# Optimization experiments

Measured on AMD Instinct MI355X. Metric: run time of the kernel, lower is better.

The kernel has to match this reference:

```python
import jax, jax.numpy as jnp
import numpy as np

B, T, F, H, E, CTX = 64, 400, 80, 256, 256, 20


def setup_inputs() -> dict:
    ks = iter(jax.random.split(jax.random.key(0), 40))

    def p(shape):
        return jax.random.normal(next(ks), shape, jnp.float32) * 0.1

    inp = {"x": p((B, T, F))}
    inp["emb_W"], inp["emb_b"] = p((E, F)), p((E,))
    for name, din, dh in [("e1", F, H), ("e2", H, H), ("e3", H, H),
                          ("d1", 2 * E, H), ("d2", H, H), ("d3", H, F)]:
        inp[name + "_Wih"] = p((4 * dh, din))
        inp[name + "_Whh"] = p((4 * dh, dh))
        inp[name + "_b"] = p((4 * dh,))  # fused b_ih + b_hh
    inp["key_W"], inp["key_b"] = p((E, H)), p((E,))
    inp["val_W"], inp["val_b"] = p((E, H)), p((E,))
    inp["epoch"] = 5  # unused when isTrain=False (no teacher forcing)
    return inp


def _lstm(xin, hc, Wih, Whh, b):
    h, c = hc
    g = xin @ Wih.T + h @ Whh.T + b
    i, f, gg, o = jnp.split(g, 4, axis=-1)  # torch gate order i,f,g,o
    c = jax.nn.sigmoid(f) * c + jax.nn.sigmoid(i) * jnp.tanh(gg)
    h = jax.nn.sigmoid(o) * jnp.tanh(c)
    return (h, c)


def _forward(x, emb_W, emb_b, e1_Wih, e1_Whh, e1_b, e2_Wih, e2_Whh, e2_b,
             e3_Wih, e3_Whh, e3_b, d1_Wih, d1_Whh, d1_b, d2_Wih, d2_Whh, d2_b,
             d3_Wih, d3_Whh, d3_b, key_W, key_b, val_W, val_b):
    Bb = x.shape[0]
    z = lambda d: (jnp.zeros((Bb, d), x.dtype), jnp.zeros((Bb, d), x.dtype))

    def encoder(enc, xin):
        e1, e2, e3 = enc
        e1 = _lstm(xin, e1, e1_Wih, e1_Whh, e1_b)
        e2 = _lstm(e1[0], e2, e2_Wih, e2_Whh, e2_b)
        e3 = _lstm(e2[0], e3, e3_Wih, e3_Whh, e3_b)
        k = e3[0] @ key_W.T + key_b
        v = e3[0] @ val_W.T + val_b
        return (e1, e2, e3), k, v

    def decoder(dec, emb, ctx):
        d1, d2, d3 = dec
        din = jnp.concatenate([emb, ctx], axis=-1)  # [B, 2E]
        d1 = _lstm(din, d1, d1_Wih, d1_Whh, d1_b)
        d2 = _lstm(d1[0], d2, d2_Wih, d2_Whh, d2_b)
        d3 = _lstm(d2[0], d3, d3_Wih, d3_Whh, d3_b)
        return (d1, d2, d3)

    # phase 1: encoder warmup over steps 0..CTX-1
    def p1(enc, xt):
        enc, k, v = encoder(enc, xt)
        return enc, (k, v)

    enc, (ks_, vs_) = jax.lax.scan(p1, (z(H), z(H), z(H)),
                                   jnp.swapaxes(x[:, :CTX], 0, 1))
    kbuf = jnp.swapaxes(ks_, 0, 1)  # [B, CTX, E]: keys for steps 0..CTX-1
    vbuf = jnp.swapaxes(vs_, 0, 1)

    # step i == CTX: first decoder step; context = current value (values[-1])
    enc, k20, v20 = encoder(enc, x[:, CTX])
    kbuf = jnp.concatenate([kbuf[:, 1:], k20[:, None]], axis=1)
    vbuf = jnp.concatenate([vbuf[:, 1:], v20[:, None]], axis=1)
    emb = x[:, CTX - 1] @ emb_W.T + emb_b
    dec = decoder((z(H), z(H), z(F)), emb, v20)
    out20 = dec[2][0]  # [B, F]

    def p2(carry, _):
        enc, dec, kbuf, vbuf, last = carry
        enc, k, v = encoder(enc, last)           # encoder_input = prev decoder out
        emb = last @ emb_W.T + emb_b             # embedding of prev decoder out
        q = dec[1][0]                            # decoder2 hidden from prev step
        attn = jax.nn.softmax(jnp.einsum('bke,be->bk', kbuf, q), axis=-1)
        ctx = jnp.einsum('bk,bke->be', attn, vbuf)
        dec = decoder(dec, emb, ctx)
        kbuf = jnp.concatenate([kbuf[:, 1:], k[:, None]], axis=1)
        vbuf = jnp.concatenate([vbuf[:, 1:], v[:, None]], axis=1)
        out = dec[2][0]
        return (enc, dec, kbuf, vbuf, out), out

    _, outs = jax.lax.scan(p2, (enc, dec, kbuf, vbuf, out20), None,
                           length=T - CTX - 1)
    # [B, T-CTX, F] = [B, 380, 80]
    return jnp.concatenate([out20[:, None], jnp.swapaxes(outs, 0, 1)], axis=1)


def reference(x, emb_W, emb_b, e1_Wih, e1_Whh, e1_b, e2_Wih, e2_Whh, e2_b,
              e3_Wih, e3_Whh, e3_b, d1_Wih, d1_Whh, d1_b, d2_Wih, d2_Whh, d2_b,
              d3_Wih, d3_Whh, d3_b, key_W, key_b, val_W, val_b, epoch):
    return _forward(x, emb_W, emb_b, e1_Wih, e1_Whh, e1_b, e2_Wih, e2_Whh, e2_b,
                    e3_Wih, e3_Whh, e3_b, d1_Wih, d1_Whh, d1_b, d2_Wih, d2_Whh,
                    d2_b, d3_Wih, d3_Whh, d3_b, key_W, key_b, val_W, val_b)
```

## Files before the change

### kernel.cpp

```cpp
#include <hip/hip_runtime.h>

typedef short bf16x8 __attribute__((ext_vector_type(8)));
typedef float f32x4 __attribute__((ext_vector_type(4)));

#define DEV static __device__ __forceinline__
#define SCOPE_AGENT __HIP_MEMORY_SCOPE_AGENT

DEV unsigned short f2bf(float f) {
  unsigned u = __float_as_uint(f);
  unsigned r = u + 0x7fffu + ((u >> 16) & 1u);
  return (unsigned short)(r >> 16);
}
DEV float bf2f(unsigned short h) { return __uint_as_float(((unsigned)h) << 16); }
DEV void f2hilo(float f, unsigned short& hi, unsigned short& lo) {
  hi = f2bf(f);
  lo = f2bf(f - bf2f(hi));
}
DEV float sigm(float x) { return 1.f / (1.f + __expf(-x)); }
DEV float tanh_(float x) {
  x = fminf(15.f, fmaxf(-15.f, x));
  float e = __expf(2.f * x);
  return (e - 1.f) / (e + 1.f);
}

DEV void st_sc_u16(unsigned short* p, unsigned short v) {
  __hip_atomic_store(p, v, __ATOMIC_RELAXED, SCOPE_AGENT);
}
DEV void st_sc_f32(float* p, float v) {
  __hip_atomic_store(p, v, __ATOMIC_RELAXED, SCOPE_AGENT);
}
DEV void st_sc_u64(unsigned long long* p, unsigned long long v) {
  __hip_atomic_store(p, v, __ATOMIC_RELAXED, SCOPE_AGENT);
}
DEV unsigned long long ld_sc_u64(const unsigned long long* p) {
  return __hip_atomic_load((unsigned long long*)p, __ATOMIC_RELAXED, SCOPE_AGENT);
}
DEV unsigned ld_sc_u32(const unsigned* p) {
  return __hip_atomic_load((unsigned*)p, __ATOMIC_RELAXED, SCOPE_AGENT);
}
DEV void vm_drain() { asm volatile("s_waitcnt vmcnt(0)" ::: "memory"); }

constexpr size_t WE1 = 1024 * 352, WE2 = 1024 * 512, WE3 = 1024 * 512,
                 WD1 = 1024 * 768, WD2 = 1024 * 512, WD3 = 320 * 352,
                 WKEY = 256 * 256, WVAL = 256 * 256, WEMB = 256 * 96;
constexpr size_t E1HI = 0, E1LO = E1HI + WE1, E2HI = E1LO + WE1, E2LO = E2HI + WE2,
                 E3HI = E2LO + WE2, E3LO = E3HI + WE3, D1HI = E3LO + WE3, D1LO = D1HI + WD1,
                 D2HI = D1LO + WD1, D2LO = D2HI + WD2, D3HI = D2LO + WD2, D3LO = D3HI + WD3,
                 KHI = D3LO + WD3, KLO = KHI + WKEY, VHI = KLO + WKEY, VLO = VHI + WVAL,
                 EMHI = VLO + WVAL, EMLO = EMHI + WEMB, WTOT = EMLO + WEMB;

constexpr size_t XPAD_ELEMS = (size_t)400 * 64 * 96;
constexpr size_t XPAD_HI_B = WTOT * 2;
constexpr size_t XPAD_LO_B = XPAD_HI_B + XPAD_ELEMS * 2;
constexpr size_t STATE_B = XPAD_LO_B + XPAD_ELEMS * 2;

constexpr size_t H256_SZB = (size_t)2 * 2 * 64 * 256 * 2;
constexpr size_t HE1 = 0, HE2 = H256_SZB, HE3 = 2 * H256_SZB, HD1 = 3 * H256_SZB,
                 HD2 = 4 * H256_SZB;
constexpr size_t HLAST = 5 * H256_SZB;
constexpr size_t HLAST_SZB = (size_t)2 * 2 * 64 * 96 * 2;
constexpr size_t BARO = HLAST + HLAST_SZB;
constexpr size_t STATE_BYTES = BARO + 9 * 400 * 4 + 64;

constexpr size_t RINGK_B = STATE_B + STATE_BYTES;
constexpr size_t RING_SZ = (size_t)22 * 64 * 256 * 4;
constexpr size_t RINGV_B = RINGK_B + RING_SZ;
constexpr size_t CTXH_B = RINGV_B + RING_SZ;
constexpr size_t CTXL_B = CTXH_B + (size_t)64 * 256 * 2;
constexpr size_t D1BP_B = CTXL_B + (size_t)64 * 256 * 2;
constexpr size_t WS_NEED = D1BP_B + 4096;

#define LE1 0
#define LE2 1
#define LE3 2
#define LKS 3
#define LAT 5
#define LD1 6
#define LD2 7
#define LD3 8

constexpr int NWG = 59;
constexpr int WGS = 256;

__global__ void prep_w(const float* __restrict__ wih, int din, const float* __restrict__ whh,
                       int dh, int rows, int dinp, int kp, unsigned short* __restrict__ whi,
                       unsigned short* __restrict__ wlo) {
  size_t idx = (size_t)blockIdx.x * 256 + threadIdx.x;
  size_t tot = (size_t)rows * kp;
  if (idx >= tot) return;
  int j = (int)(idx / kp), k = (int)(idx % kp);
  float v = 0.f;
  if (k < dinp) {
    if (k < din) v = wih[(size_t)j * din + k];
  } else {
    int k2 = k - dinp;
    if (k2 < dh) v = whh[(size_t)j * dh + k2];
  }
  unsigned short hi, lo;
  f2hilo(v, hi, lo);
  whi[idx] = hi;
  wlo[idx] = lo;
}

__global__ void prep_d1_w(const float* __restrict__ wih, const float* __restrict__ whh,
                          const float* __restrict__ embW, unsigned short* __restrict__ whi,
                          unsigned short* __restrict__ wlo) {
  size_t idx = (size_t)blockIdx.x * 256 + threadIdx.x;
  constexpr size_t tot = (size_t)1024 * 608;
  if (idx >= tot) return;
  int j = (int)(idx / 608), f = (int)(idx % 608);
  float v = 0.f;
  if (f < 96) {
    if (f < 80) {
      const float* wr = wih + (size_t)j * 512;
#pragma unroll 4
      for (int m = 0; m < 256; m++) v += wr[m] * embW[(size_t)m * 80 + f];
    }
  } else if (f < 352) {
    v = wih[(size_t)j * 512 + 256 + (f - 96)];
  } else {
    v = whh[(size_t)j * 256 + (f - 352)];
  }
  unsigned short hi, lo;
  f2hilo(v, hi, lo);
  whi[idx] = hi;
  wlo[idx] = lo;
}

__global__ void prep_d1_bias(const float* __restrict__ wih, const float* __restrict__ embb,
                             const float* __restrict__ d1b, float* __restrict__ out) {
  int j = blockIdx.x * 256 + threadIdx.x;
  if (j >= 1024) return;
  float v = d1b[j];
  const float* wr = wih + (size_t)j * 512;
#pragma unroll 4
  for (int m = 0; m < 256; m++) v += wr[m] * embb[m];
  out[j] = v;
}

__global__ void prep_x(const float* __restrict__ x, unsigned short* __restrict__ xh,
                       unsigned short* __restrict__ xl) {
  size_t idx = (size_t)blockIdx.x * 256 + threadIdx.x;
  if (idx >= XPAD_ELEMS) return;
  int t = (int)(idx / 6144), rbf = (int)(idx % 6144), b = rbf / 96, f = rbf % 96;
  float v = (f < 80) ? x[(size_t)b * 32000 + (size_t)t * 80 + f] : 0.f;
  unsigned short hi, lo;
  f2hilo(v, hi, lo);
  xh[idx] = hi;
  xl[idx] = lo;
}


template <int COLS, int STRIDE>
DEV void copy_hl(unsigned short* lds, const unsigned short* hi, const unsigned short* lo,
                 int tid) {
  constexpr int CU64 = COLS / 4;
  constexpr int PER = 64 * CU64;
  constexpr int TOT = PER * 2;
  constexpr int loOff = 64 * STRIDE;
  for (int base = 0; base < TOT; base += WGS * 32) {
    unsigned long long v[32];
    int dst[32];
#pragma unroll
    for (int u = 0; u < 32; u++) {
      int i = base + u * WGS + tid;
      dst[u] = -1;
      if (i < TOT) {
        int pl = (i >= PER) ? 1 : 0;
        int j = pl ? (i - PER) : i;
        int row = j / CU64, cc = j - row * CU64;
        const unsigned long long* s = (const unsigned long long*)(pl ? lo : hi);
        v[u] = ld_sc_u64(s + j);
        dst[u] = (pl ? loOff : 0) + row * STRIDE + ((cc * 4) ^ ((row & 7) << 3));
      }
    }
#pragma unroll
    for (int u = 0; u < 32; u++)
      if (dst[u] >= 0) *(unsigned long long*)(lds + dst[u]) = v[u];
  }
}

DEV void mfma3(f32x4& acc, bf16x8 ah, bf16x8 al, bf16x8 bh, bf16x8 bl) {
  acc = __builtin_amdgcn_mfma_f32_16x16x32_bf16(ah, bh, acc, 0, 0, 0);
  acc = __builtin_amdgcn_mfma_f32_16x16x32_bf16(al, bh, acc, 0, 0, 0);
  acc = __builtin_amdgcn_mfma_f32_16x16x32_bf16(ah, bl, acc, 0, 0, 0);
}

DEV void zacc44(f32x4 (&a)[4][4]) {
#pragma unroll
  for (int g = 0; g < 4; g++)
#pragma unroll
    for (int m = 0; m < 4; m++) a[g][m] = f32x4{0.f, 0.f, 0.f, 0.f};
}

template <int STRIDE>
DEV void mfma_range(const unsigned short* lds, int lane, int ut, int H,
                    const unsigned short* __restrict__ Whi,
                    const unsigned short* __restrict__ Wlo, int Kp, int kwOff, int kbLo,
                    int kbHi, f32x4 (&acc)[4][4]) {
  const int col = lane & 15, kg = lane >> 4;
  constexpr int loOff = 64 * STRIDE;
  for (int kb = kbLo; kb < kbHi; kb++) {
    const int ka = kb * 32 + kg * 8;
    bf16x8 ah[4], al[4];
#pragma unroll
    for (int m = 0; m < 4; m++) {
      int row = m * 16 + col;
      int off = row * STRIDE + (ka ^ ((row & 7) << 3));
      ah[m] = *(const bf16x8*)(lds + off);
      al[m] = *(const bf16x8*)(lds + loOff + off);
    }
#pragma unroll
    for (int g = 0; g < 4; g++) {
      size_t wr = (size_t)(g * H + ut * 16 + col) * Kp + kwOff + ka;
      bf16x8 bh = *(const bf16x8*)(Whi + wr);
      bf16x8 bl = *(const bf16x8*)(Wlo + wr);
#pragma unroll
      for (int m = 0; m < 4; m++) mfma3(acc[g][m], ah[m], al[m], bh, bl);
    }
  }
}

template <int COLS, int STRIDE>
DEV void chunk_pass(unsigned short* lds, const unsigned short* hi, const unsigned short* lo,
                    int tid, int lane, int ut, int utActive, int H,
                    const unsigned short* __restrict__ Whi,
                    const unsigned short* __restrict__ Wlo, int Kp, int kwOff, int half,
                    f32x4 (&acc)[4][4]) {
  __syncthreads();
  copy_hl<COLS, STRIDE>(lds, hi, lo, tid);
  __syncthreads();
  constexpr int NKB = COLS / 32;
  const int lo_kb = half ? (NKB + 1) / 2 : 0;
  const int hi_kb = half ? NKB : (NKB + 1) / 2;
  if (utActive) mfma_range<STRIDE>(lds, lane, ut, H, Whi, Wlo, Kp, kwOff, lo_kb, hi_kb, acc);
}

DEV void reduce_pair(unsigned short* lds, int lane, int pair, int half, f32x4 (&acc)[4][4]) {
  float* red = (float*)lds;
  const int base = (pair * 64 + lane) * 68;
  __syncthreads();
  if (half) {
#pragma unroll
    for (int g = 0; g < 4; g++)
#pragma unroll
      for (int m = 0; m < 4; m++)
#pragma unroll
        for (int r = 0; r < 4; r++) red[base + (g * 4 + m) * 4 + r] = acc[g][m][r];
  }
  __syncthreads();
  if (!half) {
#pragma unroll
    for (int g = 0; g < 4; g++)
#pragma unroll
      for (int m = 0; m < 4; m++)
#pragma unroll
        for (int r = 0; r < 4; r++) acc[g][m][r] += red[base + (g * 4 + m) * 4 + r];
  }
}

DEV void cell_update(int lane, int ut, int H, int Hpad, const float* __restrict__ bias,
                     f32x4 (&acc)[4][4], float (&c)[4][4], unsigned short* hwhi,
                     unsigned short* hwlo, float* outp) {
  const int col = lane & 15, kg = lane >> 4;
  const int u = ut * 16 + col;
  const float bi = bias[u], bff = bias[H + u], bg = bias[2 * H + u], bo = bias[3 * H + u];
#pragma unroll
  for (int m = 0; m < 4; m++)
#pragma unroll
    for (int r = 0; r < 4; r++) {
      int b = m * 16 + kg * 4 + r;
      float gi = acc[0][m][r] + bi, gf = acc[1][m][r] + bff;
      float gg = acc[2][m][r] + bg, go = acc[3][m][r] + bo;
      float cn = sigm(gf) * c[m][r] + sigm(gi) * tanh_(gg);
      float hh = sigm(go) * tanh_(cn);
      c[m][r] = cn;
      unsigned short hi, lo;
      f2hilo(hh, hi, lo);
      st_sc_u16(hwhi + b * Hpad + u, hi);
      st_sc_u16(hwlo + b * Hpad + u, lo);
      if (outp) outp[(size_t)b * 30400 + u] = hh;
    }
}

DEV void spin3(const unsigned* p0, unsigned t0, const unsigned* p1, unsigned t1,
               const unsigned* p2, unsigned t2) {
  for (;;) {
    unsigned a = p0 ? ld_sc_u32(p0) : 0xFFFFFFFFu;
    unsigned b = p1 ? ld_sc_u32(p1) : 0xFFFFFFFFu;
    unsigned c = p2 ? ld_sc_u32(p2) : 0xFFFFFFFFu;
    if (a >= t0 && b >= t1 && c >= t2) return;
    __builtin_amdgcn_s_sleep(1);
  }
}

__global__ void __launch_bounds__(WGS, 1)
seq_main(const float* e1b, const float* e2b, const float* e3b, const float* d2b,
         const float* d3b, const float* keyb, const float* valb, float* dout,
         unsigned char* ws) {
  __shared__ unsigned short lds_s[32768];
  unsigned short* lds = lds_s;

  const int wg = blockIdx.x, tid = threadIdx.x;
  const int wv = tid >> 6, lane = tid & 63;
  const int pair = wv >> 1, half = wv & 1;

  unsigned short* W = (unsigned short*)ws;
  const unsigned short* xh = (const unsigned short*)(ws + XPAD_HI_B);
  const unsigned short* xl = (const unsigned short*)(ws + XPAD_LO_B);
  unsigned char* st = ws + STATE_B;
  float* ringk = (float*)(ws + RINGK_B);
  float* ringv = (float*)(ws + RINGV_B);
  unsigned short* ctxh = (unsigned short*)(ws + CTXH_B);
  unsigned short* ctxl = (unsigned short*)(ws + CTXL_B);
  const float* d1bp = (const float*)(ws + D1BP_B);
  unsigned* C = (unsigned*)(st + BARO);
  auto CNT = [&](int l, int tt) { return C + l * 400 + tt; };

  auto hb = [&](size_t off, int par, int hl, int Hpad) {
    return (unsigned short*)(st + off) + (size_t)(par * 2 + hl) * 64 * Hpad;
  };
  auto bump = [&](int l, int tt) {
    if (tid == 0) __hip_atomic_fetch_add(CNT(l, tt), 1u, __ATOMIC_RELAXED, SCOPE_AGENT);
  };

  if (wg < 8) {
    const int ut = wg * 2 + pair;
    float c[4][4] = {{0.f}};
    for (int t = 0; t < 400; ++t) {
      const int p = t & 1, q = p ^ 1;
      f32x4 acc[4][4];
      zacc44(acc);
      if (tid == 0 && t >= 1) spin3(CNT(LE1, t - 1), 8, nullptr, 0, nullptr, 0);
      chunk_pass<256, 256>(lds, hb(HE1, q, 0, 256), hb(HE1, q, 1, 256), tid, lane, ut, 1, 256,
                           W + E1HI, W + E1LO, 352, 96, half, acc);
      if (tid == 0)
        spin3(t >= 21 ? CNT(LD3, t - 1) : nullptr, 3, t >= 2 ? CNT(LE2, t - 2) : nullptr, 8,
              nullptr, 0);
      if (t <= 20)
        chunk_pass<96, 128>(lds, xh + (size_t)t * 6144, xl + (size_t)t * 6144, tid, lane, ut, 1,
                            256, W + E1HI, W + E1LO, 352, 0, half, acc);
      else
        chunk_pass<96, 128>(lds, hb(HLAST, q, 0, 96), hb(HLAST, q, 1, 96), tid, lane, ut, 1,
                            256, W + E1HI, W + E1LO, 352, 0, half, acc);
      reduce_pair(lds, lane, pair, half, acc);
      if (!half)
        cell_update(lane, ut, 256, 256, e1b, acc, c, hb(HE1, p, 0, 256), hb(HE1, p, 1, 256),
                    nullptr);
      vm_drain();
      __syncthreads();
      bump(LE1, t);
    }
  } else if (wg < 16) {
    const int ut = (wg - 8) * 2 + pair;
    float c[4][4] = {{0.f}};
    for (int t = 0; t < 400; ++t) {
      const int p = t & 1, q = p ^ 1;
      f32x4 acc[4][4];
      zacc44(acc);
      if (tid == 0 && t >= 1) spin3(CNT(LE2, t - 1), 8, nullptr, 0, nullptr, 0);
      chunk_pass<256, 256>(lds, hb(HE2, q, 0, 256), hb(HE2, q, 1, 256), tid, lane, ut, 1, 256,
                           W + E2HI, W + E2LO, 512, 256, half, acc);
      if (tid == 0)
        spin3(CNT(LE1, t), 8, t >= 2 ? CNT(LE3, t - 2) : nullptr, 8, nullptr, 0);
      chunk_pass<256, 256>(lds, hb(HE1, p, 0, 256), hb(HE1, p, 1, 256), tid, lane, ut, 1, 256,
                           W + E2HI, W + E2LO, 512, 0, half, acc);
      reduce_pair(lds, lane, pair, half, acc);
      if (!half)
        cell_update(lane, ut, 256, 256, e2b, acc, c, hb(HE2, p, 0, 256), hb(HE2, p, 1, 256),
                    nullptr);
      vm_drain();
      __syncthreads();
      bump(LE2, t);
    }
  } else if (wg < 24) {
    const int ut = (wg - 16) * 2 + pair;
    float c[4][4] = {{0.f}};
    for (int t = 0; t < 400; ++t) {
      const int p = t & 1, q = p ^ 1;
      f32x4 acc[4][4];
      zacc44(acc);
      if (tid == 0 && t >= 1) spin3(CNT(LE3, t - 1), 8, nullptr, 0, nullptr, 0);
      chunk_pass<256, 256>(lds, hb(HE3, q, 0, 256), hb(HE3, q, 1, 256), tid, lane, ut, 1, 256,
                           W + E3HI, W + E3LO, 512, 256, half, acc);
      if (tid == 0) spin3(CNT(LE2, t), 8, nullptr, 0, nullptr, 0);
      chunk_pass<256, 256>(lds, hb(HE2, p, 0, 256), hb(HE2, p, 1, 256), tid, lane, ut, 1, 256,
                           W + E3HI, W + E3LO, 512, 0, half, acc);
      reduce_pair(lds, lane, pair, half, acc);
      if (tid == 0 && t >= 1) spin3(CNT(LKS, t - 1), 16, nullptr, 0, nullptr, 0);
      __syncthreads();
      if (!half)
        cell_update(lane, ut, 256, 256, e3b, acc, c, hb(HE3, p, 0, 256), hb(HE3, p, 1, 256),
                    nullptr);
      vm_drain();
      __syncthreads();
      bump(LE3, t);
    }
  } else if (wg < 40) {
    const int b0 = (wg - 24) * 4;
    float* kvx = (float*)(lds + 8192);
    for (int t = 0; t < 400; ++t) {
      const int s = (t <= 20) ? t : t - 1;
      const int ps = s & 1;
      const bool doKV = (t != 21);
      if (doKV) {
        if (tid == 0) spin3(CNT(LE3, s), 8, nullptr, 0, nullptr, 0);
        __syncthreads();
        for (int i = tid; i < 512; i += WGS) {
          int pl = i >> 8, j = i & 255, row = j >> 6, cc = j & 63;
          const unsigned long long* srcp =
              (const unsigned long long*)hb(HE3, ps, pl, 256) + (size_t)(b0 + row) * 64 + cc;
          unsigned long long v = ld_sc_u64(srcp);
          *(unsigned long long*)(lds + pl * 4096 + row * 256 +
                                 ((cc * 4) ^ ((row & 7) << 3))) = v;
        }
        __syncthreads();
      }
      bump(LKS, t);
      if (doKV) {
        const int slot = s % 22;
        const int col = lane & 15, kg = lane >> 4;
        for (int jj = 0; jj < 8; ++jj) {
          int jt = wv * 8 + jj;
          bool isK = jt < 16;
          int j = (isK ? jt : jt - 16) * 16 + col;
          const unsigned short* Whi = W + (isK ? KHI : VHI);
          const unsigned short* Wlo = W + (isK ? KLO : VLO);
          f32x4 acc = f32x4{0.f, 0.f, 0.f, 0.f};
          for (int kb = 0; kb < 8; kb++) {
            int ka = kb * 32 + kg * 8;
            int offA = col * 256 + (ka ^ ((col & 7) << 3));
            bf16x8 ah = *(const bf16x8*)(lds + offA);
            bf16x8 al = *(const bf16x8*)(lds + 4096 + offA);
            size_t wr = (size_t)j * 256 + ka;
            bf16x8 bh = *(const bf16x8*)(Whi + wr);
            bf16x8 bl = *(const bf16x8*)(Wlo + wr);
            mfma3(acc, ah, al, bh, bl);
          }
          if (kg == 0) {
            float bj = (isK ? keyb : valb)[j];
            float* ringp = (isK ? ringk : ringv) + (size_t)slot * 64 * 256;
#pragma unroll
            for (int r = 0; r < 4; r++) {
              float v = acc[r] + bj;
              st_sc_f32(ringp + (size_t)(b0 + r) * 256 + j, v);
              kvx[r * 512 + (isK ? j : 256 + j)] = v;
            }
          }
        }
        __syncthreads();
      }
      if (t == 20) {
        float f[4];
#pragma unroll
        for (int j = 0; j < 4; j++) f[j] = kvx[wv * 512 + 256 + lane * 4 + j];
        unsigned short hi[4], lo[4];
#pragma unroll
        for (int j = 0; j < 4; j++) f2hilo(f[j], hi[j], lo[j]);
        unsigned long long ph = (unsigned long long)hi[0] | ((unsigned long long)hi[1] << 16) |
                                ((unsigned long long)hi[2] << 32) |
                                ((unsigned long long)hi[3] << 48);
        unsigned long long pl = (unsigned long long)lo[0] | ((unsigned long long)lo[1] << 16) |
                                ((unsigned long long)lo[2] << 32) |
                                ((unsigned long long)lo[3] << 48);
        st_sc_u64((unsigned long long*)(ctxh + (b0 + wv) * 256 + lane * 4), ph);
        st_sc_u64((unsigned long long*)(ctxl + (b0 + wv) * 256 + lane * 4), pl);
      } else if (t >= 21) {
        if (tid == 0) spin3(CNT(LD2, t - 1), 8, CNT(LD1, t - 1), 8, nullptr, 0);
        __syncthreads();
        const int b = b0 + wv;
        const int qp = (t & 1) ^ 1;
        const unsigned short* qh = hb(HD2, qp, 0, 256);
        const unsigned short* ql = hb(HD2, qp, 1, 256);
        unsigned long long hq = ld_sc_u64((const unsigned long long*)(qh + b * 256 + lane * 4));
        unsigned long long lq = ld_sc_u64((const unsigned long long*)(ql + b * 256 + lane * 4));
        float qv[4];
#pragma unroll
        for (int j = 0; j < 4; j++)
          qv[j] = bf2f((unsigned short)(hq >> (16 * j))) + bf2f((unsigned short)(lq >> (16 * j)));
        float sArr[20];
#pragma unroll
        for (int i = 0; i < 19; i++) {
          int slot = (t - 20 + i) % 22;
          const unsigned long long* kp =
              (const unsigned long long*)(ringk + ((size_t)slot * 64 + b) * 256 + lane * 4);
          unsigned long long k0 = ld_sc_u64(kp), k1 = ld_sc_u64(kp + 1);
          sArr[i] = __uint_as_float((unsigned)k0) * qv[0] +
                    __uint_as_float((unsigned)(k0 >> 32)) * qv[1] +
                    __uint_as_float((unsigned)k1) * qv[2] +
                    __uint_as_float((unsigned)(k1 >> 32)) * qv[3];
        }
        {
          float acc19 = 0.f;
#pragma unroll
          for (int j = 0; j < 4; j++) acc19 += kvx[wv * 512 + lane * 4 + j] * qv[j];
          sArr[19] = acc19;
        }
#pragma unroll
        for (int off = 32; off >= 1; off >>= 1)
#pragma unroll
          for (int i = 0; i < 20; i++) sArr[i] += __shfl_xor(sArr[i], off, 64);
        float mx = sArr[0];
#pragma unroll
        for (int i = 1; i < 20; i++) mx = fmaxf(mx, sArr[i]);
        float den = 0.f;
#pragma unroll
        for (int i = 0; i < 20; i++) {
          sArr[i] = __expf(sArr[i] - mx);
          den += sArr[i];
        }
        float inv = 1.f / den;
        float a0 = 0.f, a1 = 0.f, a2 = 0.f, a3 = 0.f;
#pragma unroll
        for (int i = 0; i < 19; i++) {
          int slot = (t - 20 + i) % 22;
          const unsigned long long* vp =
              (const unsigned long long*)(ringv + ((size_t)slot * 64 + b) * 256 + lane * 4);
          unsigned long long v0 = ld_sc_u64(vp), v1 = ld_sc_u64(vp + 1);
          a0 += sArr[i] * __uint_as_float((unsigned)v0);
          a1 += sArr[i] * __uint_as_float((unsigned)(v0 >> 32));
          a2 += sArr[i] * __uint_as_float((unsigned)v1);
          a3 += sArr[i] * __uint_as_float((unsigned)(v1 >> 32));
        }
        a0 += sArr[19] * kvx[wv * 512 + 256 + lane * 4 + 0];
        a1 += sArr[19] * kvx[wv * 512 + 256 + lane * 4 + 1];
        a2 += sArr[19] * kvx[wv * 512 + 256 + lane * 4 + 2];
        a3 += sArr[19] * kvx[wv * 512 + 256 + lane * 4 + 3];
        float f[4] = {a0 * inv, a1 * inv, a2 * inv, a3 * inv};
        unsigned short hi[4], lo[4];
#pragma unroll
        for (int j = 0; j < 4; j++) f2hilo(f[j], hi[j], lo[j]);
        unsigned long long ph = (unsigned long long)hi[0] | ((unsigned long long)hi[1] << 16) |
                                ((unsigned long long)hi[2] << 32) |
                                ((unsigned long long)hi[3] << 48);
        unsigned long long pl = (unsigned long long)lo[0] | ((unsigned long long)lo[1] << 16) |
                                ((unsigned long long)lo[2] << 32) |
                                ((unsigned long long)lo[3] << 48);
        st_sc_u64((unsigned long long*)(ctxh + b * 256 + lane * 4), ph);
        st_sc_u64((unsigned long long*)(ctxl + b * 256 + lane * 4), pl);
      }
      vm_drain();
      __syncthreads();
      bump(LAT, t);
    }
  } else if (wg < 48) {
    const int ut = (wg - 40) * 2 + pair;
    float c[4][4] = {{0.f}};
    for (int t = 20; t < 400; ++t) {
      const int p = t & 1, q = p ^ 1;
      f32x4 acc[4][4];
      zacc44(acc);
      if (tid == 0 && t >= 21) spin3(CNT(LD1, t - 1), 8, nullptr, 0, nullptr, 0);
      chunk_pass<256, 256>(lds, hb(HD1, q, 0, 256), hb(HD1, q, 1, 256), tid, lane, ut, 1, 256,
                           W + D1HI, W + D1LO, 608, 352, half, acc);
      if (tid == 0 && t >= 21) spin3(CNT(LD3, t - 1), 3, nullptr, 0, nullptr, 0);
      if (t == 20)
        chunk_pass<96, 128>(lds, xh + (size_t)19 * 6144, xl + (size_t)19 * 6144, tid, lane, ut,
                            1, 256, W + D1HI, W + D1LO, 608, 0, half, acc);
      else
        chunk_pass<96, 128>(lds, hb(HLAST, q, 0, 96), hb(HLAST, q, 1, 96), tid, lane, ut, 1,
                            256, W + D1HI, W + D1LO, 608, 0, half, acc);
      if (tid == 0) spin3(CNT(LAT, t), 16, nullptr, 0, nullptr, 0);
      chunk_pass<256, 256>(lds, ctxh, ctxl, tid, lane, ut, 1, 256, W + D1HI, W + D1LO, 608, 96,
                           half, acc);
      reduce_pair(lds, lane, pair, half, acc);
      if (!half)
        cell_update(lane, ut, 256, 256, d1bp, acc, c, hb(HD1, p, 0, 256), hb(HD1, p, 1, 256),
                    nullptr);
      vm_drain();
      __syncthreads();
      bump(LD1, t);
    }
  } else if (wg < 56) {
    const int ut = (wg - 48) * 2 + pair;
    float c[4][4] = {{0.f}};
    for (int t = 20; t < 400; ++t) {
      const int p = t & 1, q = p ^ 1;
      f32x4 acc[4][4];
      zacc44(acc);
      if (tid == 0 && t >= 21) spin3(CNT(LD2, t - 1), 8, nullptr, 0, nullptr, 0);
      chunk_pass<256, 256>(lds, hb(HD2, q, 0, 256), hb(HD2, q, 1, 256), tid, lane, ut, 1, 256,
                           W + D2HI, W + D2LO, 512, 256, half, acc);
      if (tid == 0) spin3(CNT(LD1, t), 8, nullptr, 0, nullptr, 0);
      chunk_pass<256, 256>(lds, hb(HD1, p, 0, 256), hb(HD1, p, 1, 256), tid, lane, ut, 1, 256,
                           W + D2HI, W + D2LO, 512, 0, half, acc);
      reduce_pair(lds, lane, pair, half, acc);
      if (!half)
        cell_update(lane, ut, 256, 256, d2b, acc, c, hb(HD2, p, 0, 256), hb(HD2, p, 1, 256),
                    nullptr);
      vm_drain();
      __syncthreads();
      bump(LD2, t);
    }
  } else {
    const int ut = (wg - 56) * 2 + pair;
    const int utActive = (ut < 5) ? 1 : 0;
    float c[4][4] = {{0.f}};
    for (int t = 20; t < 400; ++t) {
      const int p = t & 1, q = p ^ 1;
      f32x4 acc[4][4];
      zacc44(acc);
      if (tid == 0 && t >= 21) spin3(CNT(LD3, t - 1), 3, nullptr, 0, nullptr, 0);
      chunk_pass<96, 128>(lds, hb(HLAST, q, 0, 96), hb(HLAST, q, 1, 96), tid, lane, ut, utActive,
                          80, W + D3HI, W + D3LO, 352, 256, half, acc);
      if (tid == 0) spin3(CNT(LD2, t), 8, nullptr, 0, nullptr, 0);
      chunk_pass<256, 256>(lds, hb(HD2, p, 0, 256), hb(HD2, p, 1, 256), tid, lane, ut, utActive,
                           80, W + D3HI, W + D3LO, 352, 0, half, acc);
      reduce_pair(lds, lane, pair, half, acc);
      if (!half && utActive)
        cell_update(lane, ut, 80, 96, d3b, acc, c, hb(HLAST, p, 0, 96), hb(HLAST, p, 1, 96),
                    dout + (size_t)(t - 20) * 80);
      vm_drain();
      __syncthreads();
      bump(LD3, t);
    }
  }
}

extern "C" void kernel_launch(void* const* d_in, const int* in_sizes, int n_in, void* d_out,
                              int out_size, void* d_ws, size_t ws_size, hipStream_t stream) {
  if (ws_size < WS_NEED) return;

  const float* x = (const float*)d_in[0];
  const float* embW = (const float*)d_in[1];
  const float* embB = (const float*)d_in[2];
  const float* e1Wih = (const float*)d_in[3];
  const float* e1Whh = (const float*)d_in[4];
  const float* e1B = (const float*)d_in[5];
  const float* e2Wih = (const float*)d_in[6];
  const float* e2Whh = (const float*)d_in[7];
  const float* e2B = (const float*)d_in[8];
  const float* e3Wih = (const float*)d_in[9];
  const float* e3Whh = (const float*)d_in[10];
  const float* e3B = (const float*)d_in[11];
  const float* d1Wih = (const float*)d_in[12];
  const float* d1Whh = (const float*)d_in[13];
  const float* d1B = (const float*)d_in[14];
  const float* d2Wih = (const float*)d_in[15];
  const float* d2Whh = (const float*)d_in[16];
  const float* d2B = (const float*)d_in[17];
  const float* d3Wih = (const float*)d_in[18];
  const float* d3Whh = (const float*)d_in[19];
  const float* d3B = (const float*)d_in[20];
  const float* keyW = (const float*)d_in[21];
  const float* keyB = (const float*)d_in[22];
  const float* valW = (const float*)d_in[23];
  const float* valB = (const float*)d_in[24];

  unsigned char* ws = (unsigned char*)d_ws;
  unsigned short* W = (unsigned short*)ws;
  float* doutf = (float*)d_out;

  auto launch_w = [&](const float* wih, int din, const float* whh, int dh, int rows, int dinp,
                      int kp, size_t offhi, size_t offlo) {
    size_t tot = (size_t)rows * kp;
    int blocks = (int)((tot + 255) / 256);
    prep_w<<<blocks, 256, 0, stream>>>(wih, din, whh, dh, rows, dinp, kp, W + offhi, W + offlo);
  };
  launch_w(e1Wih, 80, e1Whh, 256, 1024, 96, 352, E1HI, E1LO);
  launch_w(e2Wih, 256, e2Whh, 256, 1024, 256, 512, E2HI, E2LO);
  launch_w(e3Wih, 256, e3Whh, 256, 1024, 256, 512, E3HI, E3LO);
  launch_w(d2Wih, 256, d2Whh, 256, 1024, 256, 512, D2HI, D2LO);
  launch_w(d3Wih, 256, d3Whh, 80, 320, 256, 352, D3HI, D3LO);
  launch_w(keyW, 256, nullptr, 0, 256, 256, 256, KHI, KLO);
  launch_w(valW, 256, nullptr, 0, 256, 256, 256, VHI, VLO);
  {
    size_t tot = (size_t)1024 * 608;
    prep_d1_w<<<(int)((tot + 255) / 256), 256, 0, stream>>>(d1Wih, d1Whh, embW, W + D1HI,
                                                            W + D1LO);
    prep_d1_bias<<<4, 256, 0, stream>>>(d1Wih, embB, d1B, (float*)(ws + D1BP_B));
  }
  prep_x<<<(int)((XPAD_ELEMS + 255) / 256), 256, 0, stream>>>(
      x, (unsigned short*)(ws + XPAD_HI_B), (unsigned short*)(ws + XPAD_LO_B));
  hipMemsetAsync(ws + STATE_B, 0, STATE_BYTES, stream);

  seq_main<<<dim3(NWG), dim3(WGS), 0, stream>>>(e1B, e2B, e3B, d2B, d3B, keyB, valB, doutf, ws);
}
```

Baseline: 17.10 ms.

## Fuse key/value projection partials into encoder-3 workgroups and double-buffer context

Encoder-3 workgroups now stage their new hidden slice in LDS, write it out with 64-bit stores, and compute partial key/value projections over their own 32 hidden units into a double-buffered partial buffer. The attention workgroups then only sum eight partials plus bias into the K/V ring instead of running a separate projection stage with its own LKS barrier. The context buffer is double-buffered by step parity, so attention no longer has to wait on decoder-1 before overwriting it. This shortens the serial dependency chain per timestep, at the cost of extra global traffic for the partials and more work inside the encoder-3 critical path.

```diff
diff --git a/kernel.cpp b/kernel.cpp
--- a/kernel.cpp
+++ b/kernel.cpp
@@ -2,6 +2,7 @@
 
 typedef short bf16x8 __attribute__((ext_vector_type(8)));
 typedef float f32x4 __attribute__((ext_vector_type(4)));
+typedef unsigned long long u64;
 
 #define DEV static __device__ __forceinline__
 #define SCOPE_AGENT __HIP_MEMORY_SCOPE_AGENT
@@ -29,11 +30,11 @@
 DEV void st_sc_f32(float* p, float v) {
   __hip_atomic_store(p, v, __ATOMIC_RELAXED, SCOPE_AGENT);
 }
-DEV void st_sc_u64(unsigned long long* p, unsigned long long v) {
+DEV void st_sc_u64(u64* p, u64 v) {
   __hip_atomic_store(p, v, __ATOMIC_RELAXED, SCOPE_AGENT);
 }
-DEV unsigned long long ld_sc_u64(const unsigned long long* p) {
-  return __hip_atomic_load((unsigned long long*)p, __ATOMIC_RELAXED, SCOPE_AGENT);
+DEV u64 ld_sc_u64(const u64* p) {
+  return __hip_atomic_load((u64*)p, __ATOMIC_RELAXED, SCOPE_AGENT);
 }
 DEV unsigned ld_sc_u32(const unsigned* p) {
   return __hip_atomic_load((unsigned*)p, __ATOMIC_RELAXED, SCOPE_AGENT);
@@ -66,14 +67,15 @@
 constexpr size_t RING_SZ = (size_t)22 * 64 * 256 * 4;
 constexpr size_t RINGV_B = RINGK_B + RING_SZ;
 constexpr size_t CTXH_B = RINGV_B + RING_SZ;
-constexpr size_t CTXL_B = CTXH_B + (size_t)64 * 256 * 2;
-constexpr size_t D1BP_B = CTXL_B + (size_t)64 * 256 * 2;
-constexpr size_t WS_NEED = D1BP_B + 4096;
+constexpr size_t CTXL_B = CTXH_B + (size_t)2 * 64 * 256 * 2;
+constexpr size_t D1BP_B = CTXL_B + (size_t)2 * 64 * 256 * 2;
+constexpr size_t P_B = D1BP_B + 4096;
+constexpr size_t P_SZ = (size_t)2 * 8 * 64 * 512 * 4;
+constexpr size_t WS_NEED = P_B + P_SZ;
 
 #define LE1 0
 #define LE2 1
 #define LE3 2
-#define LKS 3
 #define LAT 5
 #define LD1 6
 #define LD2 7
@@ -81,6 +83,7 @@
 
 constexpr int NWG = 59;
 constexpr int WGS = 256;
+constexpr int HSTG = 20480;
 
 __global__ void prep_w(const float* __restrict__ wih, int din, const float* __restrict__ whh,
                        int dh, int rows, int dinp, int kp, unsigned short* __restrict__ whi,
@@ -159,7 +162,7 @@
   constexpr int TOT = PER * 2;
   constexpr int loOff = 64 * STRIDE;
   for (int base = 0; base < TOT; base += WGS * 32) {
-    unsigned long long v[32];
+    u64 v[32];
     int dst[32];
 #pragma unroll
     for (int u = 0; u < 32; u++) {
@@ -169,14 +172,14 @@
         int pl = (i >= PER) ? 1 : 0;
         int j = pl ? (i - PER) : i;
         int row = j / CU64, cc = j - row * CU64;
-        const unsigned long long* s = (const unsigned long long*)(pl ? lo : hi);
+        const u64* s = (const u64*)(pl ? lo : hi);
         v[u] = ld_sc_u64(s + j);
         dst[u] = (pl ? loOff : 0) + row * STRIDE + ((cc * 4) ^ ((row & 7) << 3));
       }
     }
 #pragma unroll
     for (int u = 0; u < 32; u++)
-      if (dst[u] >= 0) *(unsigned long long*)(lds + dst[u]) = v[u];
+      if (dst[u] >= 0) *(u64*)(lds + dst[u]) = v[u];
   }
 }
 
@@ -283,6 +286,41 @@
     }
 }
 
+DEV void cell_update_lds40(unsigned short* hstage, int lane, int pairIdx, int ut, int H,
+                           const float* __restrict__ bias, f32x4 (&acc)[4][4],
+                           float (&c)[4][4]) {
+  const int col = lane & 15, kg = lane >> 4;
+  const int u = ut * 16 + col;
+  const int uloc = pairIdx * 16 + col;
+  const float bi = bias[u], bff = bias[H + u], bg = bias[2 * H + u], bo = bias[3 * H + u];
+#pragma unroll
+  for (int m = 0; m < 4; m++)
+#pragma unroll
+    for (int r = 0; r < 4; r++) {
+      int b = m * 16 + kg * 4 + r;
+      float gi = acc[0][m][r] + bi, gf = acc[1][m][r] + bff;
+      float gg = acc[2][m][r] + bg, go = acc[3][m][r] + bo;
+      float cn = sigm(gf) * c[m][r] + sigm(gi) * tanh_(gg);
+      float hh = sigm(go) * tanh_(cn);
+      c[m][r] = cn;
+      unsigned short hi, lo;
+      f2hilo(hh, hi, lo);
+      hstage[b * 40 + uloc] = hi;
+      hstage[2560 + b * 40 + uloc] = lo;
+    }
+}
+
+DEV void store_h40(const unsigned short* hstage, int tid, unsigned short* hwhi,
+                   unsigned short* hwlo, int u0) {
+  for (int i = tid; i < 1024; i += WGS) {
+    int pl = i >> 9;
+    int j = i & 511;
+    int b = j >> 3, cc = j & 7;
+    u64 v = *(const u64*)(hstage + pl * 2560 + b * 40 + cc * 4);
+    st_sc_u64((u64*)((pl ? hwlo : hwhi) + (size_t)b * 256 + u0) + cc, v);
+  }
+}
+
 DEV void spin3(const unsigned* p0, unsigned t0, const unsigned* p1, unsigned t1,
                const unsigned* p2, unsigned t2) {
   for (;;) {
@@ -314,6 +352,7 @@
   unsigned short* ctxh = (unsigned short*)(ws + CTXH_B);
   unsigned short* ctxl = (unsigned short*)(ws + CTXL_B);
   const float* d1bp = (const float*)(ws + D1BP_B);
+  float* Pbuf = (float*)(ws + P_B);
   unsigned* C = (unsigned*)(st + BARO);
   auto CNT = [&](int l, int tt) { return C + l * 400 + tt; };
 
@@ -375,6 +414,7 @@
     }
   } else if (wg < 24) {
     const int ut = (wg - 16) * 2 + pair;
+    const int u0 = (wg - 16) * 32;
     float c[4][4] = {{0.f}};
     for (int t = 0; t < 400; ++t) {
       const int p = t & 1, q = p ^ 1;
@@ -387,114 +427,120 @@
       chunk_pass<256, 256>(lds, hb(HE2, p, 0, 256), hb(HE2, p, 1, 256), tid, lane, ut, 1, 256,
                            W + E3HI, W + E3LO, 512, 0, half, acc);
       reduce_pair(lds, lane, pair, half, acc);
-      if (tid == 0 && t >= 1) spin3(CNT(LKS, t - 1), 16, nullptr, 0, nullptr, 0);
-      __syncthreads();
-      if (!half)
-        cell_update(lane, ut, 256, 256, e3b, acc, c, hb(HE3, p, 0, 256), hb(HE3, p, 1, 256),
-                    nullptr);
-      vm_drain();
-      __syncthreads();
-      bump(LE3, t);
-    }
-  } else if (wg < 40) {
-    const int b0 = (wg - 24) * 4;
-    float* kvx = (float*)(lds + 8192);
-    for (int t = 0; t < 400; ++t) {
-      const int s = (t <= 20) ? t : t - 1;
-      const int ps = s & 1;
-      const bool doKV = (t != 21);
-      if (doKV) {
-        if (tid == 0) spin3(CNT(LE3, s), 8, nullptr, 0, nullptr, 0);
-        __syncthreads();
-        for (int i = tid; i < 512; i += WGS) {
-          int pl = i >> 8, j = i & 255, row = j >> 6, cc = j & 63;
-          const unsigned long long* srcp =
-              (const unsigned long long*)hb(HE3, ps, pl, 256) + (size_t)(b0 + row) * 64 + cc;
-          unsigned long long v = ld_sc_u64(srcp);
-          *(unsigned long long*)(lds + pl * 4096 + row * 256 +
-                                 ((cc * 4) ^ ((row & 7) << 3))) = v;
+      if (tid == 0 && t >= 2 && t <= 22) spin3(CNT(LAT, t - 2), 16, nullptr, 0, nullptr, 0);
+      __syncthreads();
+      unsigned short* hstage = lds + HSTG;
+      if (!half) cell_update_lds40(hstage, lane, pair, ut, 256, e3b, acc, c);
+      __syncthreads();
+      store_h40(hstage, tid, hb(HE3, p, 0, 256), hb(HE3, p, 1, 256), u0);
+      {
+        const int col = lane & 15, kg = lane >> 4;
+        bf16x8 ah[4], al[4];
+#pragma unroll
+        for (int m = 0; m < 4; m++) {
+          ah[m] = *(const bf16x8*)(hstage + (m * 16 + col) * 40 + kg * 8);
+          al[m] = *(const bf16x8*)(hstage + 2560 + (m * 16 + col) * 40 + kg * 8);
         }
-        __syncthreads();
-      }
-      bump(LKS, t);
-      if (doKV) {
-        const int slot = s % 22;
-        const int col = lane & 15, kg = lane >> 4;
+        float* Pw = Pbuf + ((size_t)(t & 1) * 8 + (wg - 16)) * (64 * 512);
         for (int jj = 0; jj < 8; ++jj) {
           int jt = wv * 8 + jj;
           bool isK = jt < 16;
-          int j = (isK ? jt : jt - 16) * 16 + col;
-          const unsigned short* Whi = W + (isK ? KHI : VHI);
-          const unsigned short* Wlo = W + (isK ? KLO : VLO);
-          f32x4 acc = f32x4{0.f, 0.f, 0.f, 0.f};
-          for (int kb = 0; kb < 8; kb++) {
-            int ka = kb * 32 + kg * 8;
-            int offA = col * 256 + (ka ^ ((col & 7) << 3));
-            bf16x8 ah = *(const bf16x8*)(lds + offA);
-            bf16x8 al = *(const bf16x8*)(lds + 4096 + offA);
-            size_t wr = (size_t)j * 256 + ka;
-            bf16x8 bh = *(const bf16x8*)(Whi + wr);
-            bf16x8 bl = *(const bf16x8*)(Wlo + wr);
-            mfma3(acc, ah, al, bh, bl);
-          }
-          if (kg == 0) {
-            float bj = (isK ? keyb : valb)[j];
-            float* ringp = (isK ? ringk : ringv) + (size_t)slot * 64 * 256;
+          int jrow = (isK ? jt : jt - 16) * 16 + col;
+          size_t wr = (size_t)jrow * 256 + u0 + kg * 8;
+          bf16x8 bh = *(const bf16x8*)(W + (isK ? KHI : VHI) + wr);
+          bf16x8 bl = *(const bf16x8*)(W + (isK ? KLO : VLO) + wr);
+          f32x4 a4[4];
+#pragma unroll
+          for (int m = 0; m < 4; m++) a4[m] = f32x4{0.f, 0.f, 0.f, 0.f};
+#pragma unroll
+          for (int m = 0; m < 4; m++) mfma3(a4[m], ah[m], al[m], bh, bl);
+          int f = isK ? jrow : jrow + 256;
+#pragma unroll
+          for (int m = 0; m < 4; m++)
 #pragma unroll
             for (int r = 0; r < 4; r++) {
-              float v = acc[r] + bj;
-              st_sc_f32(ringp + (size_t)(b0 + r) * 256 + j, v);
-              kvx[r * 512 + (isK ? j : 256 + j)] = v;
+              int b2 = m * 16 + kg * 4 + r;
+              st_sc_f32(Pw + (size_t)b2 * 512 + f, a4[m][r]);
             }
+        }
+      }
+      vm_drain();
+      __syncthreads();
+      bump(LE3, t);
+    }
+  } else if (wg < 40) {
+    const int b0 = (wg - 24) * 4;
+    const int b = b0 + wv;
+    for (int t = 0; t < 400; ++t) {
+      const int s = (t <= 20) ? t : t - 1;
+      const bool doSum = (t != 21);
+      float v[8];
+      if (doSum) {
+        if (tid == 0) spin3(CNT(LE3, s), 8, nullptr, 0, nullptr, 0);
+        __syncthreads();
+        const int slot = s % 22;
+        const float* Pb = Pbuf + (size_t)(s & 1) * 8 * 64 * 512;
+        const int f0 = lane * 8;
+#pragma unroll
+        for (int j = 0; j < 8; j++)
+          v[j] = (f0 + j < 256) ? keyb[f0 + j] : valb[f0 + j - 256];
+        for (int w = 0; w < 8; w++) {
+          const u64* src = (const u64*)(Pb + ((size_t)w * 64 + b) * 512 + f0);
+#pragma unroll
+          for (int j2 = 0; j2 < 4; j2++) {
+            u64 d = ld_sc_u64(src + j2);
+            v[j2 * 2] += __uint_as_float((unsigned)d);
+            v[j2 * 2 + 1] += __uint_as_float((unsigned)(d >> 32));
           }
         }
+        float* ringp = (lane < 32) ? ringk : ringv;
+        int fe = (lane < 32) ? f0 : f0 - 256;
+        float* dstp = ringp + ((size_t)slot * 64 + b) * 256 + fe;
+#pragma unroll
+        for (int j2 = 0; j2 < 4; j2++) {
+          u64 d = ((u64)__float_as_uint(v[j2 * 2 + 1]) << 32) | __float_as_uint(v[j2 * 2]);
+          st_sc_u64((u64*)dstp + j2, d);
+        }
+      }
+      if (t == 20 && lane >= 32) {
+        int e = lane * 8 - 256;
+        unsigned short hi[8], lo[8];
+#pragma unroll
+        for (int j = 0; j < 8; j++) f2hilo(v[j], hi[j], lo[j]);
+        u64 ph0 = (u64)hi[0] | ((u64)hi[1] << 16) | ((u64)hi[2] << 32) | ((u64)hi[3] << 48);
+        u64 ph1 = (u64)hi[4] | ((u64)hi[5] << 16) | ((u64)hi[6] << 32) | ((u64)hi[7] << 48);
+        u64 pl0 = (u64)lo[0] | ((u64)lo[1] << 16) | ((u64)lo[2] << 32) | ((u64)lo[3] << 48);
+        u64 pl1 = (u64)lo[4] | ((u64)lo[5] << 16) | ((u64)lo[6] << 32) | ((u64)lo[7] << 48);
+        st_sc_u64((u64*)(ctxh + b * 256 + e), ph0);
+        st_sc_u64((u64*)(ctxh + b * 256 + e) + 1, ph1);
+        st_sc_u64((u64*)(ctxl + b * 256 + e), pl0);
+        st_sc_u64((u64*)(ctxl + b * 256 + e) + 1, pl1);
+      }
+      if (t >= 21) {
+        vm_drain();
+        if (tid == 0) spin3(CNT(LD2, t - 1), 8, nullptr, 0, nullptr, 0);
         __syncthreads();
-      }
-      if (t == 20) {
-        float f[4];
-#pragma unroll
-        for (int j = 0; j < 4; j++) f[j] = kvx[wv * 512 + 256 + lane * 4 + j];
-        unsigned short hi[4], lo[4];
-#pragma unroll
-        for (int j = 0; j < 4; j++) f2hilo(f[j], hi[j], lo[j]);
-        unsigned long long ph = (unsigned long long)hi[0] | ((unsigned long long)hi[1] << 16) |
-                                ((unsigned long long)hi[2] << 32) |
-                                ((unsigned long long)hi[3] << 48);
-        unsigned long long pl = (unsigned long long)lo[0] | ((unsigned long long)lo[1] << 16) |
-                                ((unsigned long long)lo[2] << 32) |
-                                ((unsigned long long)lo[3] << 48);
-        st_sc_u64((unsigned long long*)(ctxh + (b0 + wv) * 256 + lane * 4), ph);
-        st_sc_u64((unsigned long long*)(ctxl + (b0 + wv) * 256 + lane * 4), pl);
-      } else if (t >= 21) {
-        if (tid == 0) spin3(CNT(LD2, t - 1), 8, CNT(LD1, t - 1), 8, nullptr, 0);
-        __syncthreads();
-        const int b = b0 + wv;
+        unsigned short* ch = ctxh + (size_t)(t & 1) * 64 * 256;
+        unsigned short* cl = ctxl + (size_t)(t & 1) * 64 * 256;
         const int qp = (t & 1) ^ 1;
         const unsigned short* qh = hb(HD2, qp, 0, 256);
         const unsigned short* ql = hb(HD2, qp, 1, 256);
-        unsigned long long hq = ld_sc_u64((const unsigned long long*)(qh + b * 256 + lane * 4));
-        unsigned long long lq = ld_sc_u64((const unsigned long long*)(ql + b * 256 + lane * 4));
+        u64 hq = ld_sc_u64((const u64*)(qh + b * 256 + lane * 4));
+        u64 lq = ld_sc_u64((const u64*)(ql + b * 256 + lane * 4));
         float qv[4];
 #pragma unroll
         for (int j = 0; j < 4; j++)
           qv[j] = bf2f((unsigned short)(hq >> (16 * j))) + bf2f((unsigned short)(lq >> (16 * j)));
         float sArr[20];
 #pragma unroll
-        for (int i = 0; i < 19; i++) {
+        for (int i = 0; i < 20; i++) {
           int slot = (t - 20 + i) % 22;
-          const unsigned long long* kp =
-              (const unsigned long long*)(ringk + ((size_t)slot * 64 + b) * 256 + lane * 4);
-          unsigned long long k0 = ld_sc_u64(kp), k1 = ld_sc_u64(kp + 1);
+          const u64* kp = (const u64*)(ringk + ((size_t)slot * 64 + b) * 256 + lane * 4);
+          u64 k0 = ld_sc_u64(kp), k1 = ld_sc_u64(kp + 1);
           sArr[i] = __uint_as_float((unsigned)k0) * qv[0] +
                     __uint_as_float((unsigned)(k0 >> 32)) * qv[1] +
                     __uint_as_float((unsigned)k1) * qv[2] +
                     __uint_as_float((unsigned)(k1 >> 32)) * qv[3];
-        }
-        {
-          float acc19 = 0.f;
-#pragma unroll
-          for (int j = 0; j < 4; j++) acc19 += kvx[wv * 512 + lane * 4 + j] * qv[j];
-          sArr[19] = acc19;
         }
 #pragma unroll
         for (int off = 32; off >= 1; off >>= 1)
@@ -512,32 +558,23 @@
         float inv = 1.f / den;
         float a0 = 0.f, a1 = 0.f, a2 = 0.f, a3 = 0.f;
 #pragma unroll
-        for (int i = 0; i < 19; i++) {
+        for (int i = 0; i < 20; i++) {
           int slot = (t - 20 + i) % 22;
-          const unsigned long long* vp =
-              (const unsigned long long*)(ringv + ((size_t)slot * 64 + b) * 256 + lane * 4);
-          unsigned long long v0 = ld_sc_u64(vp), v1 = ld_sc_u64(vp + 1);
+          const u64* vp = (const u64*)(ringv + ((size_t)slot * 64 + b) * 256 + lane * 4);
+          u64 v0 = ld_sc_u64(vp), v1 = ld_sc_u64(vp + 1);
           a0 += sArr[i] * __uint_as_float((unsigned)v0);
           a1 += sArr[i] * __uint_as_float((unsigned)(v0 >> 32));
           a2 += sArr[i] * __uint_as_float((unsigned)v1);
           a3 += sArr[i] * __uint_as_float((unsigned)(v1 >> 32));
         }
-        a0 += sArr[19] * kvx[wv * 512 + 256 + lane * 4 + 0];
-        a1 += sArr[19] * kvx[wv * 512 + 256 + lane * 4 + 1];
-        a2 += sArr[19] * kvx[wv * 512 + 256 + lane * 4 + 2];
-        a3 += sArr[19] * kvx[wv * 512 + 256 + lane * 4 + 3];
         float f[4] = {a0 * inv, a1 * inv, a2 * inv, a3 * inv};
         unsigned short hi[4], lo[4];
 #pragma unroll
         for (int j = 0; j < 4; j++) f2hilo(f[j], hi[j], lo[j]);
-        unsigned long long ph = (unsigned long long)hi[0] | ((unsigned long long)hi[1] << 16) |
-                                ((unsigned long long)hi[2] << 32) |
-                                ((unsigned long long)hi[3] << 48);
-        unsigned long long pl = (unsigned long long)lo[0] | ((unsigned long long)lo[1] << 16) |
-                                ((unsigned long long)lo[2] << 32) |
-                                ((unsigned long long)lo[3] << 48);
-        st_sc_u64((unsigned long long*)(ctxh + b * 256 + lane * 4), ph);
-        st_sc_u64((unsigned long long*)(ctxl + b * 256 + lane * 4), pl);
+        u64 ph = (u64)hi[0] | ((u64)hi[1] << 16) | ((u64)hi[2] << 32) | ((u64)hi[3] << 48);
+        u64 pl = (u64)lo[0] | ((u64)lo[1] << 16) | ((u64)lo[2] << 32) | ((u64)lo[3] << 48);
+        st_sc_u64((u64*)(ch + b * 256 + lane * 4), ph);
+        st_sc_u64((u64*)(cl + b * 256 + lane * 4), pl);
       }
       vm_drain();
       __syncthreads();
@@ -561,8 +598,8 @@
         chunk_pass<96, 128>(lds, hb(HLAST, q, 0, 96), hb(HLAST, q, 1, 96), tid, lane, ut, 1,
                             256, W + D1HI, W + D1LO, 608, 0, half, acc);
       if (tid == 0) spin3(CNT(LAT, t), 16, nullptr, 0, nullptr, 0);
-      chunk_pass<256, 256>(lds, ctxh, ctxl, tid, lane, ut, 1, 256, W + D1HI, W + D1LO, 608, 96,
-                           half, acc);
+      chunk_pass<256, 256>(lds, ctxh + (size_t)p * 64 * 256, ctxl + (size_t)p * 64 * 256, tid,
+                           lane, ut, 1, 256, W + D1HI, W + D1LO, 608, 96, half, acc);
       reduce_pair(lds, lane, pair, half, acc);
       if (!half)
         cell_update(lane, ut, 256, 256, d1bp, acc, c, hb(HD1, p, 0, 256), hb(HD1, p, 1, 256),
```

Measured after the change: 15.52 ms. -9.3%, faster.
